# Performance work log

Measured on AMD Instinct MI355X. Metric: run time of the kernel, lower is better.

Reference implementation:

```python
import jax, jax.numpy as jnp
import numpy as np

NUM_GROUPS = 32
EPS = 1e-6


def setup_inputs() -> dict:
    key = jax.random.key(0)
    ks = jax.random.split(key, 8)
    B, H, W, C = 2, 64, 64, 512
    heads, hd = 8, 64
    s = 0.02
    return {
        "x": jax.random.normal(ks[0], (B, H, W, C), jnp.float32),
        "gn_scale": jnp.ones((C,), jnp.float32),
        "gn_bias": jnp.zeros((C,), jnp.float32),
        "wq": jax.random.normal(ks[1], (C, heads, hd), jnp.float32) * s,
        "bq": jnp.zeros((heads, hd), jnp.float32),
        "wk": jax.random.normal(ks[2], (C, heads, hd), jnp.float32) * s,
        "bk": jnp.zeros((heads, hd), jnp.float32),
        "wv": jax.random.normal(ks[3], (C, heads, hd), jnp.float32) * s,
        "bv": jnp.zeros((heads, hd), jnp.float32),
        "wo": jax.random.normal(ks[4], (heads, hd, C), jnp.float32) * s,
        "bo": jnp.zeros((C,), jnp.float32),
    }


def _group_norm(x, scale, bias):
    # flax GroupNorm defaults: 32 groups, eps=1e-6, reduce over spatial + within-group channels
    B, H, W, C = x.shape
    g = NUM_GROUPS
    xg = x.reshape(B, H, W, g, C // g)
    mean = jnp.mean(xg, axis=(1, 2, 4), keepdims=True)
    var = jnp.mean(jnp.square(xg - mean), axis=(1, 2, 4), keepdims=True)
    xn = (xg - mean) * jax.lax.rsqrt(var + EPS)
    return xn.reshape(B, H, W, C) * scale + bias


def reference(x, gn_scale, gn_bias, wq, bq, wk, bk, wv, bv, wo, bo):
    B, H, W, C = x.shape
    hd = wq.shape[-1]
    h = _group_norm(x.astype(jnp.float32), gn_scale, gn_bias).astype(x.dtype)
    h = h.reshape(B, H * W, C)  # [B, S, C]
    q = jnp.einsum("bsc,chd->bshd", h, wq) + bq
    k = jnp.einsum("bsc,chd->bshd", h, wk) + bk
    v = jnp.einsum("bsc,chd->bshd", h, wv) + bv
    # standard scaled dot-product attention (head-split in source is mathematically identical)
    logits = jnp.einsum("bqhd,bkhd->bhqk", q * (hd ** -0.5), k)  # [B, h, S, S]
    attn = jax.nn.softmax(logits, axis=-1)
    o = jnp.einsum("bhqk,bkhd->bqhd", attn, v).astype(jnp.float32)
    out = jnp.einsum("bshd,hdc->bsc", o, wo) + bo
    return x + out.reshape(B, H, W, C)
```

## Files before the change

kernel.cpp:

```cpp
#include <hip/hip_runtime.h>
#include <hip/hip_bf16.h>

typedef __attribute__((ext_vector_type(8))) short bf16x8;
typedef __attribute__((ext_vector_type(4))) float f32x4;
typedef __attribute__((ext_vector_type(16))) float f32x16;

#define MFMA16(a, b, c) __builtin_amdgcn_mfma_f32_16x16x32_bf16(a, b, c, 0, 0, 0)
#define MFMA32(a, b, c) __builtin_amdgcn_mfma_f32_32x32x16_bf16(a, b, c, 0, 0, 0)

static constexpr int Bn = 2;
static constexpr int S  = 4096;
static constexpr int C  = 512;
static constexpr int NH = 8;
static constexpr int HD = 64;
static constexpr int M  = Bn * S;

#define QSCALE 0.18033688f

__device__ __forceinline__ ushort f2bf(float f) {
  unsigned u = __builtin_bit_cast(unsigned, f);
  u += 0x7fffu + ((u >> 16) & 1u);
  return (ushort)(u >> 16);
}

__device__ __forceinline__ unsigned pkbf(float a, float b) {
  return (unsigned)f2bf(a) | ((unsigned)f2bf(b) << 16);
}

__device__ __forceinline__ unsigned cvtpk(float a, float b) {
  unsigned r;
  asm("v_cvt_pk_bf16_f32 %0, %1, %2" : "=v"(r) : "v"(a), "v"(b));
  return r;
}

#define GLOAD_LDS16(g, l) __builtin_amdgcn_global_load_lds( \
    (const __attribute__((address_space(1))) unsigned*)(const void*)(g), \
    (__attribute__((address_space(3))) unsigned*)(void*)(l), 16, 0, 0)

__global__ __launch_bounds__(256) void prep_kernel(const float* __restrict__ x,
                                                   float2* __restrict__ stats,
                                                   const float* __restrict__ w0,
                                                   const float* __restrict__ w1,
                                                   const float* __restrict__ w2,
                                                   const float* __restrict__ w3,
                                                   ushort* __restrict__ wT) {
  __shared__ float tile[64][65];
  __shared__ float2 red[4];
  if (blockIdx.x < 64) {
    int bg = blockIdx.x;
    int b = bg >> 5, g = bg & 31;
    const float* xp = x + (size_t)b * S * C + g * 16;
    float sum = 0.f, sq = 0.f;
    for (int s = threadIdx.x; s < S; s += 256) {
      const float4* p = (const float4*)(xp + (size_t)s * C);
      #pragma unroll
      for (int i = 0; i < 4; i++) {
        float4 v = p[i];
        sum += v.x + v.y + v.z + v.w;
        sq  += v.x * v.x + v.y * v.y + v.z * v.z + v.w * v.w;
      }
    }
    #pragma unroll
    for (int d = 1; d < 64; d <<= 1) {
      sum += __shfl_xor(sum, d);
      sq  += __shfl_xor(sq, d);
    }
    if ((threadIdx.x & 63) == 0) red[threadIdx.x >> 6] = make_float2(sum, sq);
    __syncthreads();
    if (threadIdx.x == 0) {
      float s0 = 0.f, q0 = 0.f;
      #pragma unroll
      for (int i = 0; i < 4; i++) { s0 += red[i].x; q0 += red[i].y; }
      float inv = 1.f / (float)(S * 16);
      float mean = s0 * inv;
      float var = q0 * inv - mean * mean;
      stats[bg] = make_float2(mean, rsqrtf(var + 1e-6f));
    }
  } else {
    int bid = blockIdx.x - 64;
    int mat = bid >> 6;
    int xx = bid & 63;
    const float* w = (mat == 0) ? w0 : (mat == 1) ? w1 : (mat == 2) ? w2 : w3;
    int tr = (xx >> 3) * 64;
    int tc = (xx & 7) * 64;
    int ty = threadIdx.x >> 6, tx = threadIdx.x & 63;
    #pragma unroll
    for (int i = 0; i < 16; i++) {
      int r = i * 4 + ty;
      tile[r][tx] = w[(size_t)(tr + r) * 512 + tc + tx];
    }
    __syncthreads();
    #pragma unroll
    for (int i = 0; i < 16; i++) {
      int r = i * 4 + ty;
      wT[((size_t)mat << 18) + (size_t)(tc + r) * 512 + tr + tx] = f2bf(tile[tx][r]);
    }
  }
}

__global__ __launch_bounds__(256) void gn_apply_kernel(const float* __restrict__ x,
                                                       const float* __restrict__ sc,
                                                       const float* __restrict__ bi,
                                                       const float2* __restrict__ stats,
                                                       ushort* __restrict__ h) {
  int i = blockIdx.x * 256 + threadIdx.x;
  int s = i >> 6;
  int c0 = (i & 63) << 3;
  int b = s >> 12;
  float2 st = stats[(b << 5) + (c0 >> 4)];
  const float4* xv = (const float4*)(x + (size_t)s * C + c0);
  const float4* sv = (const float4*)(sc + c0);
  const float4* bv = (const float4*)(bi + c0);
  float4 a0 = xv[0], a1 = xv[1];
  float4 s0 = sv[0], s1 = sv[1];
  float4 b0 = bv[0], b1 = bv[1];
  uint4 pk;
  pk.x = pkbf((a0.x - st.x) * st.y * s0.x + b0.x, (a0.y - st.x) * st.y * s0.y + b0.y);
  pk.y = pkbf((a0.z - st.x) * st.y * s0.z + b0.z, (a0.w - st.x) * st.y * s0.w + b0.w);
  pk.z = pkbf((a1.x - st.x) * st.y * s1.x + b1.x, (a1.y - st.x) * st.y * s1.y + b1.y);
  pk.w = pkbf((a1.z - st.x) * st.y * s1.z + b1.z, (a1.w - st.x) * st.y * s1.w + b1.w);
  *(uint4*)(h + (size_t)i * 8) = pk;
}

__global__ __launch_bounds__(256, 3) void qkv_gemm_kernel(const ushort* __restrict__ h,
                                                          const ushort* __restrict__ wT,
                                                          const float* __restrict__ bq,
                                                          const float* __restrict__ bk,
                                                          const float* __restrict__ bv,
                                                          ushort* __restrict__ qo,
                                                          ushort* __restrict__ ko,
                                                          ushort* __restrict__ vT) {
  __shared__ ushort SM[4][4096];
  const int t = threadIdx.x;
  const int l = t & 63;
  const int w = t >> 6;
  const int lr = l & 15, lg = l >> 4;
  const int m0 = blockIdx.x * 128, n0 = blockIdx.y * 128;
  const int mw = (w >> 1) * 64, nw = (w & 1) * 64;

  const ushort* Ab = h  + (size_t)m0 * C;
  const ushort* Bb = wT + (size_t)n0 * C;

  {
    GLOAD_LDS16(Ab + (size_t)(t >> 2) * C + (t & 3) * 8,           &SM[0][t * 8]);
    GLOAD_LDS16(Ab + (size_t)(64 + (t >> 2)) * C + (t & 3) * 8,    &SM[0][(t + 256 - 512) * 8 + 4096]);
    GLOAD_LDS16(Bb + (size_t)(t >> 2) * C + (t & 3) * 8,           &SM[2][t * 8]);
    GLOAD_LDS16(Bb + (size_t)(64 + (t >> 2)) * C + (t & 3) * 8,    &SM[2][(t + 256 - 512) * 8 + 4096]);
  }
  __syncthreads();

  f32x4 acc[4][4] = {};
  int buf = 0;
  for (int kt = 0; kt < 16; kt++) {
    if (kt + 1 < 16) {
      int k0 = (kt + 1) * 32;
      int nb = buf ^ 1;
      GLOAD_LDS16(Ab + (size_t)(t >> 2) * C + k0 + (t & 3) * 8,        &SM[nb][t * 8]);
      GLOAD_LDS16(Ab + (size_t)(64 + (t >> 2)) * C + k0 + (t & 3) * 8, &SM[nb][(t + 256 - 512) * 8 + 4096]);
      GLOAD_LDS16(Bb + (size_t)(t >> 2) * C + k0 + (t & 3) * 8,        &SM[2 + nb][t * 8]);
      GLOAD_LDS16(Bb + (size_t)(64 + (t >> 2)) * C + k0 + (t & 3) * 8, &SM[2 + nb][(t + 256 - 512) * 8 + 4096]);
    }
    bf16x8 af[4], bfr[4];
    #pragma unroll
    for (int i = 0; i < 2; i++) af[i]      = *(const bf16x8*)&SM[buf][(mw + i * 16 + lr) * 32 + lg * 8];
    #pragma unroll
    for (int i = 2; i < 4; i++) af[i]      = *(const bf16x8*)&SM[buf][(mw + i * 16 + lr - 128) * 32 + lg * 8 + 4096];
    #pragma unroll
    for (int i = 0; i < 2; i++) bfr[i]     = *(const bf16x8*)&SM[2 + buf][(nw + i * 16 + lr) * 32 + lg * 8];
    #pragma unroll
    for (int i = 2; i < 4; i++) bfr[i]     = *(const bf16x8*)&SM[2 + buf][(nw + i * 16 + lr - 128) * 32 + lg * 8 + 4096];
    #pragma unroll
    for (int mi = 0; mi < 4; mi++)
      #pragma unroll
      for (int ni = 0; ni < 4; ni++)
        acc[mi][ni] = MFMA16(af[mi], bfr[ni], acc[mi][ni]);
    __syncthreads();
    buf ^= 1;
  }

  const int mat = n0 >> 9;
  const int cg0 = n0 & 511;
  if (mat == 2) {
    ushort* Tr = &SM[0][0];
    #pragma unroll
    for (int mi = 0; mi < 4; mi++) {
      #pragma unroll
      for (int ni = 0; ni < 4; ni++) {
        #pragma unroll
        for (int r = 0; r < 4; r++) {
          int s_loc = mw + mi * 16 + lg * 4 + r;
          int sp = (s_loc & ~12) | ((s_loc & 4) << 1) | ((s_loc & 8) >> 1);
          int c_loc = nw + ni * 16 + lr;
          Tr[c_loc * 128 + (sp ^ ((c_loc & 7) << 3))] = f2bf(acc[mi][ni][r] + bv[cg0 + c_loc]);
        }
      }
    }
    __syncthreads();
    const int c_loc = t >> 1, s2 = (t & 1) * 64;
    const size_t rowb = ((size_t)((m0 >> 12) * C + cg0 + c_loc)) * S + (m0 & (S - 1));
    #pragma unroll
    for (int j = 0; j < 8; j++) {
      int ch = (s2 + j * 8) ^ ((c_loc & 7) << 3);
      *(uint4*)(vT + rowb + s2 + j * 8) = *(const uint4*)&Tr[c_loc * 128 + ch];
    }
  } else {
    #pragma unroll
    for (int mi = 0; mi < 4; mi++) {
      #pragma unroll
      for (int ni = 0; ni < 4; ni++) {
        #pragma unroll
        for (int r = 0; r < 4; r++) {
          int srow = m0 + mw + mi * 16 + lg * 4 + r;
          int nl = cg0 + nw + ni * 16 + lr;
          float v = acc[mi][ni][r];
          if (mat == 0) {
            qo[(size_t)srow * C + nl] = f2bf((v + bq[nl]) * QSCALE);
          } else {
            ko[(size_t)srow * C + nl] = f2bf(v + bk[nl]);
          }
        }
      }
    }
  }
}

__global__ __launch_bounds__(256, 2) void attn_kernel(const ushort* __restrict__ q,
                                                      const ushort* __restrict__ k,
                                                      const ushort* __restrict__ vT,
                                                      ushort* __restrict__ o) {
  __shared__ ushort Kt[2][64 * 64];
  __shared__ ushort Vt[2][64 * 64];

  const int l = threadIdx.x & 63;
  const int wid = threadIdx.x >> 6;
  const int l31 = l & 31;
  const int hi = l >> 5;
  const int bh = blockIdx.y;
  const int b = bh >> 3, hh = bh & 7;
  const int q0 = blockIdx.x * 128 + wid * 32;
  constexpr int NT = S / 64;

  const ushort* qp = q + ((size_t)(b * S + q0)) * C + hh * HD;
  const ushort* kp = k + ((size_t)(b * S)) * C + hh * HD;
  const ushort* vp = vT + ((size_t)(b * C) + hh * HD) * S;

  const int srow = wid * 16 + (l >> 3);
  const int sc   = l & 7;
  const int swz8 = (sc ^ (srow & 7)) * 8;
  const ushort* kpA = kp + (size_t)srow * C + swz8;
  const ushort* kpB = kpA + (size_t)8 * C;
  const ushort* vpA = vp + (size_t)srow * S + swz8;
  const ushort* vpB = vpA + (size_t)8 * S;
  const int ldsA = (wid * 2 + 0) * 512;
  const int ldsB = (wid * 2 + 1) * 512;

  bf16x8 qa[4];
  #pragma unroll
  for (int kd = 0; kd < 4; kd++)
    qa[kd] = *(const bf16x8*)(qp + (size_t)l31 * C + kd * 16 + hi * 8);

  f32x16 oacc[2] = {};
  float lst = 0.f;

#define ATTN_STAGE(BUF, T) { \
    GLOAD_LDS16(kpA + (size_t)(T) * (64 * C), &Kt[BUF][ldsA]); \
    GLOAD_LDS16(kpB + (size_t)(T) * (64 * C), &Kt[BUF][ldsB]); \
    GLOAD_LDS16(vpA + (T) * 64, &Vt[BUF][ldsA]); \
    GLOAD_LDS16(vpB + (T) * 64, &Vt[BUF][ldsB]); \
  }

#define ATTN_COMPUTE(BUF) \
  _Pragma("unroll") \
  for (int kn = 0; kn < 2; kn++) { \
    __builtin_amdgcn_s_setprio(1); \
    f32x16 s = {}; \
    _Pragma("unroll") \
    for (int kd = 0; kd < 4; kd++) { \
      bf16x8 kf = *(const bf16x8*)&Kt[BUF][(kn * 32 + l31) * 64 + (((kd * 2 + hi) ^ (l31 & 7)) * 8)]; \
      s = MFMA32(kf, qa[kd], s); \
    } \
    __builtin_amdgcn_s_setprio(0); \
    float e[16]; \
    _Pragma("unroll") \
    for (int r = 0; r < 16; r++) e[r] = __builtin_amdgcn_exp2f(s[r]); \
    unsigned pw[8]; \
    _Pragma("unroll") \
    for (int j = 0; j < 8; j++) pw[j] = cvtpk(e[2 * j], e[2 * j + 1]); \
    lst += ((((e[0] + e[1]) + (e[2] + e[3])) + ((e[4] + e[5]) + (e[6] + e[7]))) \
          + (((e[8] + e[9]) + (e[10] + e[11])) + ((e[12] + e[13]) + (e[14] + e[15])))); \
    __builtin_amdgcn_s_setprio(1); \
    _Pragma("unroll") \
    for (int kc = 0; kc < 2; kc++) { \
      union { unsigned u[4]; bf16x8 v; } pu; \
      pu.u[0] = pw[kc * 4 + 0]; pu.u[1] = pw[kc * 4 + 1]; \
      pu.u[2] = pw[kc * 4 + 2]; pu.u[3] = pw[kc * 4 + 3]; \
      _Pragma("unroll") \
      for (int nd = 0; nd < 2; nd++) { \
        bf16x8 vf = *(const bf16x8*)&Vt[BUF][(nd * 32 + l31) * 64 + ((((kn * 2 + kc) * 2 + hi) ^ (l31 & 7)) * 8)]; \
        oacc[nd] = MFMA32(pu.v, vf, oacc[nd]); \
      } \
    } \
    __builtin_amdgcn_s_setprio(0); \
  }

  ATTN_STAGE(0, 0);
  __syncthreads();

  for (int t2 = 0; t2 < NT; t2 += 2) {
    if (t2 + 1 < NT) ATTN_STAGE(1, t2 + 1);
    ATTN_COMPUTE(0);
    __syncthreads();
    if (t2 + 2 < NT) ATTN_STAGE(0, t2 + 2);
    ATTN_COMPUTE(1);
    __syncthreads();
  }

#undef ATTN_STAGE
#undef ATTN_COMPUTE

  float lfull = lst + __shfl_xor(lst, 32);
  #pragma unroll
  for (int r = 0; r < 16; r++) {
    int row = (r & 3) + 8 * (r >> 2) + 4 * hi;
    float inv = 1.0f / __shfl(lfull, row);
    size_t base = ((size_t)(b * S + q0 + row)) * C + hh * HD;
    o[base + l31]      = f2bf(oacc[0][r] * inv);
    o[base + 32 + l31] = f2bf(oacc[1][r] * inv);
  }
}

__global__ __launch_bounds__(256, 3) void oproj_gemm_kernel(const ushort* __restrict__ o,
                                                            const ushort* __restrict__ woT,
                                                            const float* __restrict__ x,
                                                            const float* __restrict__ bo,
                                                            float* __restrict__ out) {
  __shared__ ushort As[2][128 * 32];
  __shared__ ushort Bs[2][128 * 32];
  const int t = threadIdx.x;
  const int l = t & 63;
  const int w = t >> 6;
  const int lr = l & 15, lg = l >> 4;
  const int m0 = blockIdx.x * 128, n0 = blockIdx.y * 128;
  const int mw = (w >> 1) * 64, nw = (w & 1) * 64;

  const ushort* Ab = o   + (size_t)m0 * C;
  const ushort* Bb = woT + (size_t)n0 * C;

  {
    GLOAD_LDS16(Ab + (size_t)(t >> 2) * C + (t & 3) * 8,           &As[0][t * 8]);
    GLOAD_LDS16(Ab + (size_t)(64 + (t >> 2)) * C + (t & 3) * 8,    &As[0][(t + 256) * 8]);
    GLOAD_LDS16(Bb + (size_t)(t >> 2) * C + (t & 3) * 8,           &Bs[0][t * 8]);
    GLOAD_LDS16(Bb + (size_t)(64 + (t >> 2)) * C + (t & 3) * 8,    &Bs[0][(t + 256) * 8]);
  }
  __syncthreads();

  f32x4 acc[4][4] = {};
  int buf = 0;
  for (int kt = 0; kt < 16; kt++) {
    if (kt + 1 < 16) {
      int k0 = (kt + 1) * 32;
      GLOAD_LDS16(Ab + (size_t)(t >> 2) * C + k0 + (t & 3) * 8,        &As[buf ^ 1][t * 8]);
      GLOAD_LDS16(Ab + (size_t)(64 + (t >> 2)) * C + k0 + (t & 3) * 8, &As[buf ^ 1][(t + 256) * 8]);
      GLOAD_LDS16(Bb + (size_t)(t >> 2) * C + k0 + (t & 3) * 8,        &Bs[buf ^ 1][t * 8]);
      GLOAD_LDS16(Bb + (size_t)(64 + (t >> 2)) * C + k0 + (t & 3) * 8, &Bs[buf ^ 1][(t + 256) * 8]);
    }
    bf16x8 af[4], bfr[4];
    #pragma unroll
    for (int i = 0; i < 4; i++) af[i]  = *(const bf16x8*)&As[buf][(mw + i * 16 + lr) * 32 + lg * 8];
    #pragma unroll
    for (int i = 0; i < 4; i++) bfr[i] = *(const bf16x8*)&Bs[buf][(nw + i * 16 + lr) * 32 + lg * 8];
    #pragma unroll
    for (int mi = 0; mi < 4; mi++)
      #pragma unroll
      for (int ni = 0; ni < 4; ni++)
        acc[mi][ni] = MFMA16(af[mi], bfr[ni], acc[mi][ni]);
    __syncthreads();
    buf ^= 1;
  }

  #pragma unroll
  for (int mi = 0; mi < 4; mi++) {
    #pragma unroll
    for (int ni = 0; ni < 4; ni++) {
      #pragma unroll
      for (int r = 0; r < 4; r++) {
        int srow = m0 + mw + mi * 16 + lg * 4 + r;
        int c = n0 + nw + ni * 16 + lr;
        out[(size_t)srow * C + c] = x[(size_t)srow * C + c] + acc[mi][ni][r] + bo[c];
      }
    }
  }
}

extern "C" void kernel_launch(void* const* d_in, const int* in_sizes, int n_in,
                              void* d_out, int out_size, void* d_ws, size_t ws_size,
                              hipStream_t stream) {
  const float* x  = (const float*)d_in[0];
  const float* gs = (const float*)d_in[1];
  const float* gb = (const float*)d_in[2];
  const float* wq = (const float*)d_in[3];
  const float* bq = (const float*)d_in[4];
  const float* wk = (const float*)d_in[5];
  const float* bk = (const float*)d_in[6];
  const float* wv = (const float*)d_in[7];
  const float* bv = (const float*)d_in[8];
  const float* wo = (const float*)d_in[9];
  const float* bo = (const float*)d_in[10];

  char* ws = (char*)d_ws;
  ushort* h    = (ushort*)(ws);
  ushort* wT   = (ushort*)(ws + 8388608);
  ushort* qb   = (ushort*)(ws + 10485760);
  ushort* kb   = (ushort*)(ws + 18874368);
  ushort* vTb  = (ushort*)(ws + 27262976);
  float2* st   = (float2*)(ws + 44040192);
  ushort* ofin = qb;

  prep_kernel<<<320, 256, 0, stream>>>(x, st, wq, wk, wv, wo, wT);
  gn_apply_kernel<<<2048, 256, 0, stream>>>(x, gs, gb, st, h);
  qkv_gemm_kernel<<<dim3(64, 12), 256, 0, stream>>>(h, wT, bq, bk, bv, qb, kb, vTb);
  attn_kernel<<<dim3(32, 16), 256, 0, stream>>>(qb, kb, vTb, ofin);
  oproj_gemm_kernel<<<dim3(64, 4), 256, 0, stream>>>(ofin, wT + 786432, x, bo, (float*)d_out);
}
```

Baseline: 154.0 us.

## Split attention key range across two warp groups per block and merge partials

Each attention block now has 512 threads: two groups of four waves each process half of the key sequence for the same 128 queries, with separate double-buffered LDS tiles. Partial outputs and row sums from the second half are exchanged through LDS and combined by the first group before normalization. This doubles the waves in flight per query tile to hide latency better on a grid of 512 blocks. In exchange it costs a bf16 round-trip of partial accumulators, an extra barrier, and higher LDS use per block. The softmax has no max subtraction, so the partials add directly.

```diff
diff --git a/kernel.cpp b/kernel.cpp
--- a/kernel.cpp
+++ b/kernel.cpp
@@ -21,6 +21,10 @@
   unsigned u = __builtin_bit_cast(unsigned, f);
   u += 0x7fffu + ((u >> 16) & 1u);
   return (ushort)(u >> 16);
+}
+
+__device__ __forceinline__ float bf2f(ushort u) {
+  return __builtin_bit_cast(float, (unsigned)u << 16);
 }
 
 __device__ __forceinline__ unsigned pkbf(float a, float b) {
@@ -224,35 +228,40 @@
   }
 }
 
-__global__ __launch_bounds__(256, 2) void attn_kernel(const ushort* __restrict__ q,
+__global__ __launch_bounds__(512, 4) void attn_kernel(const ushort* __restrict__ q,
                                                       const ushort* __restrict__ k,
                                                       const ushort* __restrict__ vT,
                                                       ushort* __restrict__ o) {
-  __shared__ ushort Kt[2][64 * 64];
-  __shared__ ushort Vt[2][64 * 64];
+  __shared__ ushort KtF[2][2][64 * 64];
+  __shared__ ushort VtF[2][2][64 * 64];
 
   const int l = threadIdx.x & 63;
   const int wid = threadIdx.x >> 6;
+  const int khalf = wid >> 2;
+  const int wq = wid & 3;
   const int l31 = l & 31;
   const int hi = l >> 5;
   const int bh = blockIdx.y;
   const int b = bh >> 3, hh = bh & 7;
-  const int q0 = blockIdx.x * 128 + wid * 32;
-  constexpr int NT = S / 64;
+  const int q0 = blockIdx.x * 128 + wq * 32;
+  const int k0 = khalf * (S / 2);
+  constexpr int NT = (S / 2) / 64;
 
   const ushort* qp = q + ((size_t)(b * S + q0)) * C + hh * HD;
-  const ushort* kp = k + ((size_t)(b * S)) * C + hh * HD;
-  const ushort* vp = vT + ((size_t)(b * C) + hh * HD) * S;
-
-  const int srow = wid * 16 + (l >> 3);
+  const ushort* kp = k + ((size_t)(b * S + k0)) * C + hh * HD;
+  const ushort* vp = vT + ((size_t)(b * C) + hh * HD) * S + k0;
+
+  const int srow = wq * 16 + (l >> 3);
   const int sc   = l & 7;
   const int swz8 = (sc ^ (srow & 7)) * 8;
   const ushort* kpA = kp + (size_t)srow * C + swz8;
   const ushort* kpB = kpA + (size_t)8 * C;
   const ushort* vpA = vp + (size_t)srow * S + swz8;
   const ushort* vpB = vpA + (size_t)8 * S;
-  const int ldsA = (wid * 2 + 0) * 512;
-  const int ldsB = (wid * 2 + 1) * 512;
+  const int ldsA = (wq * 2 + 0) * 512;
+  const int ldsB = (wq * 2 + 1) * 512;
+  ushort* Kg = &KtF[khalf][0][0];
+  ushort* Vg = &VtF[khalf][0][0];
 
   bf16x8 qa[4];
   #pragma unroll
@@ -263,10 +272,10 @@
   float lst = 0.f;
 
 #define ATTN_STAGE(BUF, T) { \
-    GLOAD_LDS16(kpA + (size_t)(T) * (64 * C), &Kt[BUF][ldsA]); \
-    GLOAD_LDS16(kpB + (size_t)(T) * (64 * C), &Kt[BUF][ldsB]); \
-    GLOAD_LDS16(vpA + (T) * 64, &Vt[BUF][ldsA]); \
-    GLOAD_LDS16(vpB + (T) * 64, &Vt[BUF][ldsB]); \
+    GLOAD_LDS16(kpA + (size_t)(T) * (64 * C), Kg + (BUF) * 4096 + ldsA); \
+    GLOAD_LDS16(kpB + (size_t)(T) * (64 * C), Kg + (BUF) * 4096 + ldsB); \
+    GLOAD_LDS16(vpA + (T) * 64, Vg + (BUF) * 4096 + ldsA); \
+    GLOAD_LDS16(vpB + (T) * 64, Vg + (BUF) * 4096 + ldsB); \
   }
 
 #define ATTN_COMPUTE(BUF) \
@@ -276,7 +285,7 @@
     f32x16 s = {}; \
     _Pragma("unroll") \
     for (int kd = 0; kd < 4; kd++) { \
-      bf16x8 kf = *(const bf16x8*)&Kt[BUF][(kn * 32 + l31) * 64 + (((kd * 2 + hi) ^ (l31 & 7)) * 8)]; \
+      bf16x8 kf = *(const bf16x8*)&Kg[(BUF) * 4096 + (kn * 32 + l31) * 64 + (((kd * 2 + hi) ^ (l31 & 7)) * 8)]; \
       s = MFMA32(kf, qa[kd], s); \
     } \
     __builtin_amdgcn_s_setprio(0); \
@@ -296,7 +305,7 @@
       pu.u[2] = pw[kc * 4 + 2]; pu.u[3] = pw[kc * 4 + 3]; \
       _Pragma("unroll") \
       for (int nd = 0; nd < 2; nd++) { \
-        bf16x8 vf = *(const bf16x8*)&Vt[BUF][(nd * 32 + l31) * 64 + ((((kn * 2 + kc) * 2 + hi) ^ (l31 & 7)) * 8)]; \
+        bf16x8 vf = *(const bf16x8*)&Vg[(BUF) * 4096 + (nd * 32 + l31) * 64 + ((((kn * 2 + kc) * 2 + hi) ^ (l31 & 7)) * 8)]; \
         oacc[nd] = MFMA32(pu.v, vf, oacc[nd]); \
       } \
     } \
@@ -318,14 +327,32 @@
 #undef ATTN_STAGE
 #undef ATTN_COMPUTE
 
+  ushort* Xo = &KtF[0][0][0];
+  float*  Xl = (float*)&VtF[0][0][0];
   float lfull = lst + __shfl_xor(lst, 32);
-  #pragma unroll
-  for (int r = 0; r < 16; r++) {
-    int row = (r & 3) + 8 * (r >> 2) + 4 * hi;
-    float inv = 1.0f / __shfl(lfull, row);
-    size_t base = ((size_t)(b * S + q0 + row)) * C + hh * HD;
-    o[base + l31]      = f2bf(oacc[0][r] * inv);
-    o[base + 32 + l31] = f2bf(oacc[1][r] * inv);
+
+  if (khalf == 1) {
+    if (hi == 0) Xl[wq * 32 + l31] = lfull;
+    #pragma unroll
+    for (int r = 0; r < 16; r++) {
+      int row = (r & 3) + 8 * (r >> 2) + 4 * hi;
+      Xo[(wq * 32 + row) * 64 + l31]      = f2bf(oacc[0][r]);
+      Xo[(wq * 32 + row) * 64 + 32 + l31] = f2bf(oacc[1][r]);
+    }
+  }
+  __syncthreads();
+  if (khalf == 0) {
+    float ltot = lfull + Xl[wq * 32 + l31];
+    #pragma unroll
+    for (int r = 0; r < 16; r++) {
+      int row = (r & 3) + 8 * (r >> 2) + 4 * hi;
+      float inv = 1.0f / __shfl(ltot, row);
+      float o0 = oacc[0][r] + bf2f(Xo[(wq * 32 + row) * 64 + l31]);
+      float o1 = oacc[1][r] + bf2f(Xo[(wq * 32 + row) * 64 + 32 + l31]);
+      size_t base = ((size_t)(b * S + q0 + row)) * C + hh * HD;
+      o[base + l31]      = f2bf(o0 * inv);
+      o[base + 32 + l31] = f2bf(o1 * inv);
+    }
   }
 }
 
@@ -419,6 +446,6 @@
   prep_kernel<<<320, 256, 0, stream>>>(x, st, wq, wk, wv, wo, wT);
   gn_apply_kernel<<<2048, 256, 0, stream>>>(x, gs, gb, st, h);
   qkv_gemm_kernel<<<dim3(64, 12), 256, 0, stream>>>(h, wT, bq, bk, bv, qb, kb, vTb);
-  attn_kernel<<<dim3(32, 16), 256, 0, stream>>>(qb, kb, vTb, ofin);
+  attn_kernel<<<dim3(32, 16), 512, 0, stream>>>(qb, kb, vTb, ofin);
   oproj_gemm_kernel<<<dim3(64, 4), 256, 0, stream>>>(ofin, wT + 786432, x, bo, (float*)d_out);
 }
```

New measurement: 150.2 us. 2.5% less time.
